# Performance work log

Hardware: AMD Instinct MI355X
Metric: run time of the kernel (lower is better)

Reference implementation:

```python
import jax, jax.numpy as jnp
import numpy as np

N_NODES = 100000
N_EDGES = 1600000
IN_DIM = 128
HID = 128
N_CLASSES = 16
N_GRAPHS = 512


def setup_inputs() -> dict:
    key = jax.random.key(0)
    ks = jax.random.split(key, 16)
    d = {
        "x": jax.random.normal(ks[0], (N_NODES, IN_DIM), jnp.float32),
        "src": jax.random.randint(ks[1], (N_EDGES,), 0, N_NODES, jnp.int64 if jax.config.jax_enable_x64 else jnp.int32),
        "dst": jax.random.randint(ks[2], (N_EDGES,), 0, N_NODES, jnp.int64 if jax.config.jax_enable_x64 else jnp.int32),
        "gid": jnp.sort(jax.random.randint(ks[3], (N_NODES,), 0, N_GRAPHS, jnp.int64 if jax.config.jax_enable_x64 else jnp.int32)),
    }
    s = 1.0 / np.sqrt(HID)
    for i, k in zip(range(1, 5), ks[4:8]):
        d[f"W{i}"] = jax.random.uniform(k, (HID, HID), jnp.float32, -s, s)
        d[f"b{i}"] = jnp.zeros((HID,), jnp.float32)
    d["Wv"] = jax.random.uniform(ks[8], (HID, 1), jnp.float32, -s, s)
    d["bv"] = jnp.zeros((1,), jnp.float32)
    d["Wc"] = jax.random.uniform(ks[9], (HID, N_CLASSES), jnp.float32, -s, s)
    d["bc"] = jnp.zeros((N_CLASSES,), jnp.float32)
    return d


def _gcn_layer(h, W, b, src, dst, norm_src, norm_dst):
    # DGL GraphConv, norm='both': D_dst^{-1/2} * A * D_src^{-1/2} * h * W + b, then ReLU outside
    m = (h * norm_src[:, None])[src]                                  # [E, H] edge gather
    agg = jax.ops.segment_sum(m, dst, num_segments=N_NODES)           # [N, H] scatter-add
    return jax.nn.relu(agg * norm_dst[:, None] @ W + b)


def reference(x, W1, b1, W2, b2, W3, b3, W4, b4, Wv, bv, Wc, bc, src, dst, gid):
    ones = jnp.ones((N_EDGES,), jnp.float32)
    deg_out = jnp.clip(jax.ops.segment_sum(ones, src, num_segments=N_NODES), 1.0)
    deg_in = jnp.clip(jax.ops.segment_sum(ones, dst, num_segments=N_NODES), 1.0)
    norm_src = jax.lax.rsqrt(deg_out)
    norm_dst = jax.lax.rsqrt(deg_in)

    h = _gcn_layer(x, W1, b1, src, dst, norm_src, norm_dst)
    h = _gcn_layer(h, W2, b2, src, dst, norm_src, norm_dst)
    h = _gcn_layer(h, W3, b3, src, dst, norm_src, norm_dst)
    h = _gcn_layer(h, W4, b4, src, dst, norm_src, norm_dst)

    w = jax.nn.sigmoid(h @ Wv + bv)                                   # [N, 1]
    num = jax.ops.segment_sum(h * w, gid, num_segments=N_GRAPHS)      # [G, H]
    den = jax.ops.segment_sum(w, gid, num_segments=N_GRAPHS)          # [G, 1]
    hg = jnp.where(den > 0, num / jnp.where(den > 0, den, 1.0), 0.0)  # weighted mean readout
    return hg @ Wc + bc                                               # [G, n_classes]
```

## Files before the change

kernel.cpp:

```cpp
#include <hip/hip_runtime.h>
#include <hip/hip_bf16.h>

#define N_NODES_C 100000
#define N_EDGES_C 1600000
#define HID_C 128
#define NCLS_C 16
#define NGRAPH_C 512
#define ELL_CAP 64
#define PREP_GROUPS 8
#define PREP_RANGE ((N_NODES_C + PREP_GROUPS - 1) / PREP_GROUPS)
#define PREP_GB 256
#define PREP_CHUNK (N_EDGES_C / PREP_GB)

__global__ __launch_bounds__(256) void k_prep(
    const int* __restrict__ src, const int* __restrict__ dst,
    int* cnt_out, int* cursor, int* __restrict__ ell) {
  int grp = blockIdx.x & (PREP_GROUPS - 1);
  int gb = blockIdx.x >> 3;
  int lo = grp * PREP_RANGE;
  int e0 = gb * PREP_CHUNK;
  int e1 = e0 + PREP_CHUNK;
  for (int i = e0 + threadIdx.x; i < e1; i += 256) {
    int s = src[i];
    int d = dst[i];
    if ((unsigned)(s - lo) < (unsigned)PREP_RANGE) atomicAdd(&cnt_out[s], 1);
    if ((unsigned)(d - lo) < (unsigned)PREP_RANGE) {
      int p = atomicAdd(&cursor[d], 1);
      if (p < ELL_CAP) ell[((size_t)d << 6) + p] = s;
    }
  }
}

__global__ void k_gstart(const int* __restrict__ gid, int* __restrict__ gstart) {
  int n = blockIdx.x * blockDim.x + threadIdx.x;
  if (n >= N_NODES_C) return;
  int g = gid[n];
  int gp = (n == 0) ? -1 : gid[n - 1];
  for (int k = gp + 1; k <= g; ++k) gstart[k] = n;
  if (n == N_NODES_C - 1) {
    for (int k = g + 1; k <= NGRAPH_C; ++k) gstart[k] = N_NODES_C;
  }
}

__global__ __launch_bounds__(256) void k_gemm_rowscale(
    const float* __restrict__ A, const float* __restrict__ W,
    const int* __restrict__ cnt_out, float* __restrict__ T, int rows) {
  __shared__ float sA[32][132];
  __shared__ float sB[32][132];
  int t = threadIdx.x;
  int tx = t & 15, ty = t >> 4;
  int m0 = blockIdx.x * 128;

  float acc[8][8];
#pragma unroll
  for (int i = 0; i < 8; ++i)
#pragma unroll
    for (int j = 0; j < 8; ++j) acc[i][j] = 0.f;

  int a_c4 = (t & 7) * 4;
  int a_r = t >> 3;
  int w_n4 = (t & 31) * 4;
  int w_k = t >> 5;

  for (int k0 = 0; k0 < HID_C; k0 += 32) {
#pragma unroll
    for (int rr = 0; rr < 4; ++rr) {
      int r = rr * 32 + a_r;
      int row = m0 + r;
      float4 v = make_float4(0.f, 0.f, 0.f, 0.f);
      if (row < rows) v = *(const float4*)&A[(size_t)row * HID_C + k0 + a_c4];
      sA[a_c4 + 0][r] = v.x;
      sA[a_c4 + 1][r] = v.y;
      sA[a_c4 + 2][r] = v.z;
      sA[a_c4 + 3][r] = v.w;
    }
#pragma unroll
    for (int i = 0; i < 4; ++i) {
      int kc = i * 8 + w_k;
      float4 v = *(const float4*)&W[(size_t)(k0 + kc) * HID_C + w_n4];
      *(float4*)&sB[kc][w_n4] = v;
    }
    __syncthreads();

#pragma unroll 4
    for (int kk = 0; kk < 32; ++kk) {
      float4 a0 = *(const float4*)&sA[kk][ty * 8];
      float4 a1 = *(const float4*)&sA[kk][ty * 8 + 4];
      float4 bb0 = *(const float4*)&sB[kk][tx * 8];
      float4 bb1 = *(const float4*)&sB[kk][tx * 8 + 4];
      float a[8] = {a0.x, a0.y, a0.z, a0.w, a1.x, a1.y, a1.z, a1.w};
      float b[8] = {bb0.x, bb0.y, bb0.z, bb0.w, bb1.x, bb1.y, bb1.z, bb1.w};
#pragma unroll
      for (int i = 0; i < 8; ++i)
#pragma unroll
        for (int j = 0; j < 8; ++j) acc[i][j] = fmaf(a[i], b[j], acc[i][j]);
    }
    __syncthreads();
  }

#pragma unroll
  for (int i = 0; i < 8; ++i) {
    int row = m0 + ty * 8 + i;
    if (row < rows) {
      float sc = 1.f / sqrtf(fmaxf((float)cnt_out[row], 1.f));
      float4 v0 = {acc[i][0] * sc, acc[i][1] * sc, acc[i][2] * sc, acc[i][3] * sc};
      float4 v1 = {acc[i][4] * sc, acc[i][5] * sc, acc[i][6] * sc, acc[i][7] * sc};
      float4* p = (float4*)&T[(size_t)row * HID_C + tx * 8];
      p[0] = v0;
      p[1] = v1;
    }
  }
}

__global__ __launch_bounds__(256) void k_agg(
    const float* __restrict__ T, const int* __restrict__ cnt_in,
    const int* __restrict__ ell, const float* __restrict__ bias,
    float* __restrict__ H) {
  int wid = threadIdx.x >> 6, lane = threadIdx.x & 63;
  int half = lane >> 5, li = lane & 31;
  int n = blockIdx.x * 4 + wid;
  if (n >= N_NODES_C) return;
  const int* lst = ell + ((size_t)n << 6);
  int deg = cnt_in[n];
  if (deg > ELL_CAP) deg = ELL_CAP;
  const float4* T4 = (const float4*)T;
  float4 acc = make_float4(0.f, 0.f, 0.f, 0.f);
  int e = 0;
  for (; e + 8 <= deg; e += 8) {
    int i0 = lst[e + 0 + half];
    int i1 = lst[e + 2 + half];
    int i2 = lst[e + 4 + half];
    int i3 = lst[e + 6 + half];
    float4 v0 = T4[(size_t)i0 * 32 + li];
    float4 v1 = T4[(size_t)i1 * 32 + li];
    float4 v2 = T4[(size_t)i2 * 32 + li];
    float4 v3 = T4[(size_t)i3 * 32 + li];
    acc.x += v0.x + v1.x + v2.x + v3.x;
    acc.y += v0.y + v1.y + v2.y + v3.y;
    acc.z += v0.z + v1.z + v2.z + v3.z;
    acc.w += v0.w + v1.w + v2.w + v3.w;
  }
  for (; e + 2 <= deg; e += 2) {
    int i = lst[e + half];
    float4 v = T4[(size_t)i * 32 + li];
    acc.x += v.x;
    acc.y += v.y;
    acc.z += v.z;
    acc.w += v.w;
  }
  if (e < deg) {
    int i = lst[e];
    float4 v = T4[(size_t)i * 32 + li];
    if (half == 0) {
      acc.x += v.x;
      acc.y += v.y;
      acc.z += v.z;
      acc.w += v.w;
    }
  }
  acc.x += __shfl_xor(acc.x, 32);
  acc.y += __shfl_xor(acc.y, 32);
  acc.z += __shfl_xor(acc.z, 32);
  acc.w += __shfl_xor(acc.w, 32);
  if (half == 0) {
    float nd = 1.f / sqrtf(fmaxf((float)cnt_in[n], 1.f));
    float4 bb = ((const float4*)bias)[li];
    float4 r;
    r.x = fmaxf(fmaf(acc.x, nd, bb.x), 0.f);
    r.y = fmaxf(fmaf(acc.y, nd, bb.y), 0.f);
    r.z = fmaxf(fmaf(acc.z, nd, bb.z), 0.f);
    r.w = fmaxf(fmaf(acc.w, nd, bb.w), 0.f);
    ((float4*)H)[(size_t)n * 32 + li] = r;
  }
}

__global__ __launch_bounds__(256) void k_readout(
    const float* __restrict__ H, const float* __restrict__ Wv,
    const float* __restrict__ bv, const int* __restrict__ gstart,
    const float* __restrict__ Wc, const float* __restrict__ bc,
    float* __restrict__ out) {
  int g = blockIdx.x;
  int wid = threadIdx.x >> 6, lane = threadIdx.x & 63;
  int s0 = gstart[g], s1 = gstart[g + 1];
  float2 wv2 = ((const float2*)Wv)[lane];
  float bvs = bv[0];
  float ax = 0.f, ay = 0.f, dw = 0.f;
  for (int n = s0 + wid; n < s1; n += 4) {
    float2 h2 = ((const float2*)H)[(size_t)n * 64 + lane];
    float p = h2.x * wv2.x + h2.y * wv2.y;
#pragma unroll
    for (int off = 32; off > 0; off >>= 1) p += __shfl_xor(p, off);
    float w = 1.f / (1.f + expf(-(p + bvs)));
    ax += h2.x * w;
    ay += h2.y * w;
    dw += w;
  }
  __shared__ float2 snum[4][64];
  __shared__ float sden[4];
  __shared__ float hg[HID_C];
  snum[wid][lane] = make_float2(ax, ay);
  if (lane == 0) sden[wid] = dw;
  __syncthreads();
  if (wid == 0) {
    float2 a = snum[0][lane], b = snum[1][lane], c = snum[2][lane], d = snum[3][lane];
    float den = sden[0] + sden[1] + sden[2] + sden[3];
    float inv = (den > 0.f) ? 1.f / den : 0.f;
    hg[2 * lane] = (a.x + b.x + c.x + d.x) * inv;
    hg[2 * lane + 1] = (a.y + b.y + c.y + d.y) * inv;
  }
  __syncthreads();
  if (threadIdx.x < NCLS_C) {
    int c = threadIdx.x;
    float acc = 0.f;
    for (int k = 0; k < HID_C; ++k) acc = fmaf(hg[k], Wc[k * NCLS_C + c], acc);
    out[g * NCLS_C + c] = acc + bc[c];
  }
}

extern "C" void kernel_launch(void* const* d_in, const int* in_sizes, int n_in,
                              void* d_out, int out_size, void* d_ws, size_t ws_size,
                              hipStream_t stream) {
  const float* x = (const float*)d_in[0];
  const int* src = (const int*)d_in[1];
  const int* dst = (const int*)d_in[2];
  const int* gid = (const int*)d_in[3];
  const float* W[4] = {(const float*)d_in[4], (const float*)d_in[6],
                       (const float*)d_in[8], (const float*)d_in[10]};
  const float* b[4] = {(const float*)d_in[5], (const float*)d_in[7],
                       (const float*)d_in[9], (const float*)d_in[11]};
  const float* Wv = (const float*)d_in[12];
  const float* bv = (const float*)d_in[13];
  const float* Wc = (const float*)d_in[14];
  const float* bc = (const float*)d_in[15];
  float* out = (float*)d_out;

  char* ws = (char*)d_ws;
  size_t off = 0;
  auto alloc = [&](size_t bytes) -> char* {
    char* p = ws + off;
    off = (off + bytes + 255) & ~(size_t)255;
    return p;
  };
  int* cnt_out = (int*)alloc((size_t)N_NODES_C * 4);
  int* cursor = (int*)alloc((size_t)N_NODES_C * 4);
  int* gstart = (int*)alloc((size_t)(NGRAPH_C + 1) * 4);
  int* ell = (int*)alloc((size_t)N_NODES_C * ELL_CAP * 4);
  float* tbuf = (float*)alloc((size_t)N_NODES_C * HID_C * 4);
  float* hbuf = (float*)alloc((size_t)N_NODES_C * HID_C * 4);
  (void)ws_size;
  (void)in_sizes;
  (void)n_in;
  (void)out_size;

  hipMemsetAsync(cnt_out, 0, (size_t)N_NODES_C * 4, stream);
  hipMemsetAsync(cursor, 0, (size_t)N_NODES_C * 4, stream);

  k_prep<<<PREP_GROUPS * PREP_GB, 256, 0, stream>>>(src, dst, cnt_out, cursor, ell);
  k_gstart<<<(N_NODES_C + 255) / 256, 256, 0, stream>>>(gid, gstart);

  int gemm_grid = (N_NODES_C + 127) / 128;
  int node_grid = (N_NODES_C + 3) / 4;
  const float* hin = x;
  for (int l = 0; l < 4; ++l) {
    k_gemm_rowscale<<<gemm_grid, 256, 0, stream>>>(hin, W[l], cnt_out, tbuf, N_NODES_C);
    k_agg<<<node_grid, 256, 0, stream>>>(tbuf, cursor, ell, b[l], hbuf);
    hin = hbuf;
  }

  k_readout<<<NGRAPH_C, 256, 0, stream>>>(hbuf, Wv, bv, gstart, Wc, bc, out);
}
```

Measured before the change: 825.0 us.

## Simplify edge prep, prefetch GEMM tiles, deepen gather unroll, ping-pong buffers

The edge-preparation kernel drops the node-range partitioning, so each edge is handled once by a grid-stride loop instead of being scanned by eight groups. The GEMM now loads the next k-tile of A and W into registers while computing the current one, overlapping global loads with FMAs. The aggregation loop adds a 16-neighbour unrolled stage for more memory-level parallelism and reuses the degree value already loaded. The layer loop alternates between two buffers. Possible costs are more atomic contention in prep and higher register pressure in the GEMM and gather.

```diff
diff --git a/kernel.cpp b/kernel.cpp
--- a/kernel.cpp
+++ b/kernel.cpp
@@ -7,27 +7,18 @@
 #define NCLS_C 16
 #define NGRAPH_C 512
 #define ELL_CAP 64
-#define PREP_GROUPS 8
-#define PREP_RANGE ((N_NODES_C + PREP_GROUPS - 1) / PREP_GROUPS)
-#define PREP_GB 256
-#define PREP_CHUNK (N_EDGES_C / PREP_GB)
 
 __global__ __launch_bounds__(256) void k_prep(
     const int* __restrict__ src, const int* __restrict__ dst,
     int* cnt_out, int* cursor, int* __restrict__ ell) {
-  int grp = blockIdx.x & (PREP_GROUPS - 1);
-  int gb = blockIdx.x >> 3;
-  int lo = grp * PREP_RANGE;
-  int e0 = gb * PREP_CHUNK;
-  int e1 = e0 + PREP_CHUNK;
-  for (int i = e0 + threadIdx.x; i < e1; i += 256) {
+  int i = blockIdx.x * blockDim.x + threadIdx.x;
+  int stride = gridDim.x * blockDim.x;
+  for (; i < N_EDGES_C; i += stride) {
     int s = src[i];
     int d = dst[i];
-    if ((unsigned)(s - lo) < (unsigned)PREP_RANGE) atomicAdd(&cnt_out[s], 1);
-    if ((unsigned)(d - lo) < (unsigned)PREP_RANGE) {
-      int p = atomicAdd(&cursor[d], 1);
-      if (p < ELL_CAP) ell[((size_t)d << 6) + p] = s;
-    }
+    atomicAdd(&cnt_out[s], 1);
+    int p = atomicAdd(&cursor[d], 1);
+    if (p < ELL_CAP) ell[((size_t)d << 6) + p] = s;
   }
 }
 
@@ -62,25 +53,42 @@
   int w_n4 = (t & 31) * 4;
   int w_k = t >> 5;
 
+  float4 pa[4], pw[4];
+#pragma unroll
+  for (int rr = 0; rr < 4; ++rr) {
+    int row = m0 + rr * 32 + a_r;
+    pa[rr] = make_float4(0.f, 0.f, 0.f, 0.f);
+    if (row < rows) pa[rr] = *(const float4*)&A[(size_t)row * HID_C + a_c4];
+  }
+#pragma unroll
+  for (int i = 0; i < 4; ++i)
+    pw[i] = *(const float4*)&W[(size_t)(i * 8 + w_k) * HID_C + w_n4];
+
   for (int k0 = 0; k0 < HID_C; k0 += 32) {
 #pragma unroll
     for (int rr = 0; rr < 4; ++rr) {
       int r = rr * 32 + a_r;
-      int row = m0 + r;
-      float4 v = make_float4(0.f, 0.f, 0.f, 0.f);
-      if (row < rows) v = *(const float4*)&A[(size_t)row * HID_C + k0 + a_c4];
-      sA[a_c4 + 0][r] = v.x;
-      sA[a_c4 + 1][r] = v.y;
-      sA[a_c4 + 2][r] = v.z;
-      sA[a_c4 + 3][r] = v.w;
-    }
-#pragma unroll
-    for (int i = 0; i < 4; ++i) {
-      int kc = i * 8 + w_k;
-      float4 v = *(const float4*)&W[(size_t)(k0 + kc) * HID_C + w_n4];
-      *(float4*)&sB[kc][w_n4] = v;
-    }
+      sA[a_c4 + 0][r] = pa[rr].x;
+      sA[a_c4 + 1][r] = pa[rr].y;
+      sA[a_c4 + 2][r] = pa[rr].z;
+      sA[a_c4 + 3][r] = pa[rr].w;
+    }
+#pragma unroll
+    for (int i = 0; i < 4; ++i) *(float4*)&sB[i * 8 + w_k][w_n4] = pw[i];
     __syncthreads();
+
+    if (k0 + 32 < HID_C) {
+      int kn = k0 + 32;
+#pragma unroll
+      for (int rr = 0; rr < 4; ++rr) {
+        int row = m0 + rr * 32 + a_r;
+        pa[rr] = make_float4(0.f, 0.f, 0.f, 0.f);
+        if (row < rows) pa[rr] = *(const float4*)&A[(size_t)row * HID_C + kn + a_c4];
+      }
+#pragma unroll
+      for (int i = 0; i < 4; ++i)
+        pw[i] = *(const float4*)&W[(size_t)(kn + i * 8 + w_k) * HID_C + w_n4];
+    }
 
 #pragma unroll 4
     for (int kk = 0; kk < 32; ++kk) {
@@ -121,16 +129,32 @@
   int n = blockIdx.x * 4 + wid;
   if (n >= N_NODES_C) return;
   const int* lst = ell + ((size_t)n << 6);
-  int deg = cnt_in[n];
-  if (deg > ELL_CAP) deg = ELL_CAP;
+  int degfull = cnt_in[n];
+  int deg = degfull > ELL_CAP ? ELL_CAP : degfull;
   const float4* T4 = (const float4*)T;
   float4 acc = make_float4(0.f, 0.f, 0.f, 0.f);
   int e = 0;
+  for (; e + 16 <= deg; e += 16) {
+    int i0 = lst[e + 0 + half], i1 = lst[e + 2 + half];
+    int i2 = lst[e + 4 + half], i3 = lst[e + 6 + half];
+    int i4 = lst[e + 8 + half], i5 = lst[e + 10 + half];
+    int i6 = lst[e + 12 + half], i7 = lst[e + 14 + half];
+    float4 v0 = T4[(size_t)i0 * 32 + li];
+    float4 v1 = T4[(size_t)i1 * 32 + li];
+    float4 v2 = T4[(size_t)i2 * 32 + li];
+    float4 v3 = T4[(size_t)i3 * 32 + li];
+    float4 v4 = T4[(size_t)i4 * 32 + li];
+    float4 v5 = T4[(size_t)i5 * 32 + li];
+    float4 v6 = T4[(size_t)i6 * 32 + li];
+    float4 v7 = T4[(size_t)i7 * 32 + li];
+    acc.x += v0.x + v1.x + v2.x + v3.x + v4.x + v5.x + v6.x + v7.x;
+    acc.y += v0.y + v1.y + v2.y + v3.y + v4.y + v5.y + v6.y + v7.y;
+    acc.z += v0.z + v1.z + v2.z + v3.z + v4.z + v5.z + v6.z + v7.z;
+    acc.w += v0.w + v1.w + v2.w + v3.w + v4.w + v5.w + v6.w + v7.w;
+  }
   for (; e + 8 <= deg; e += 8) {
-    int i0 = lst[e + 0 + half];
-    int i1 = lst[e + 2 + half];
-    int i2 = lst[e + 4 + half];
-    int i3 = lst[e + 6 + half];
+    int i0 = lst[e + 0 + half], i1 = lst[e + 2 + half];
+    int i2 = lst[e + 4 + half], i3 = lst[e + 6 + half];
     float4 v0 = T4[(size_t)i0 * 32 + li];
     float4 v1 = T4[(size_t)i1 * 32 + li];
     float4 v2 = T4[(size_t)i2 * 32 + li];
@@ -163,7 +187,7 @@
   acc.z += __shfl_xor(acc.z, 32);
   acc.w += __shfl_xor(acc.w, 32);
   if (half == 0) {
-    float nd = 1.f / sqrtf(fmaxf((float)cnt_in[n], 1.f));
+    float nd = 1.f / sqrtf(fmaxf((float)degfull, 1.f));
     float4 bb = ((const float4*)bias)[li];
     float4 r;
     r.x = fmaxf(fmaf(acc.x, nd, bb.x), 0.f);
@@ -245,8 +269,8 @@
   int* cursor = (int*)alloc((size_t)N_NODES_C * 4);
   int* gstart = (int*)alloc((size_t)(NGRAPH_C + 1) * 4);
   int* ell = (int*)alloc((size_t)N_NODES_C * ELL_CAP * 4);
-  float* tbuf = (float*)alloc((size_t)N_NODES_C * HID_C * 4);
-  float* hbuf = (float*)alloc((size_t)N_NODES_C * HID_C * 4);
+  float* bufA = (float*)alloc((size_t)N_NODES_C * HID_C * 4);
+  float* bufB = (float*)alloc((size_t)N_NODES_C * HID_C * 4);
   (void)ws_size;
   (void)in_sizes;
   (void)n_in;
@@ -255,17 +279,23 @@
   hipMemsetAsync(cnt_out, 0, (size_t)N_NODES_C * 4, stream);
   hipMemsetAsync(cursor, 0, (size_t)N_NODES_C * 4, stream);
 
-  k_prep<<<PREP_GROUPS * PREP_GB, 256, 0, stream>>>(src, dst, cnt_out, cursor, ell);
+  k_prep<<<2048, 256, 0, stream>>>(src, dst, cnt_out, cursor, ell);
   k_gstart<<<(N_NODES_C + 255) / 256, 256, 0, stream>>>(gid, gstart);
 
   int gemm_grid = (N_NODES_C + 127) / 128;
   int node_grid = (N_NODES_C + 3) / 4;
+
   const float* hin = x;
+  float* tcur = bufA;
+  float* hcur = bufB;
   for (int l = 0; l < 4; ++l) {
-    k_gemm_rowscale<<<gemm_grid, 256, 0, stream>>>(hin, W[l], cnt_out, tbuf, N_NODES_C);
-    k_agg<<<node_grid, 256, 0, stream>>>(tbuf, cursor, ell, b[l], hbuf);
-    hin = hbuf;
-  }
-
-  k_readout<<<NGRAPH_C, 256, 0, stream>>>(hbuf, Wv, bv, gstart, Wc, bc, out);
-}
+    k_gemm_rowscale<<<gemm_grid, 256, 0, stream>>>(hin, W[l], cnt_out, tcur, N_NODES_C);
+    k_agg<<<node_grid, 256, 0, stream>>>(tcur, cursor, ell, b[l], hcur);
+    hin = hcur;
+    float* tmp = tcur;
+    tcur = hcur;
+    hcur = tmp;
+  }
+
+  k_readout<<<NGRAPH_C, 256, 0, stream>>>(hin, Wv, bv, gstart, Wc, bc, out);
+}
```

Measured after the change: 889.8 us. 1.08x slower.
